# Kernel optimization log

Measured on AMD Instinct MI355X. Metric: run time of the kernel, lower is better.

## Reference

```python
import jax, jax.numpy as jnp
import numpy as np

D = 1024       # embedding_dim
H = 16         # num_attention_heads
B = 2
S = 2048       # seq_len == context_len


def setup_inputs() -> dict:
    key = jax.random.key(0)
    k1, k2, k3 = jax.random.split(key, 3)
    X = jax.random.normal(k1, (B, S, D), dtype=jnp.float32)
    W_qkv = jax.random.normal(k2, (D, 3 * D), dtype=jnp.float32) * 0.02
    b_qkv = jnp.zeros((3 * D,), dtype=jnp.float32)
    W_out = jax.random.normal(k3, (D, D), dtype=jnp.float32) * 0.02
    b_out = jnp.zeros((D,), dtype=jnp.float32)
    return {"X": X, "W_qkv": W_qkv, "b_qkv": b_qkv, "W_out": W_out, "b_out": b_out}


def reference(X, W_qkv, b_qkv, W_out, b_out):
    b, s, d = X.shape
    hd = d // H
    # fused QKV projection (GPT-2 Conv1D == x @ W + b)
    qkv = X @ W_qkv + b_qkv                       # [b, s, 3d]
    q, k, v = jnp.split(qkv, 3, axis=2)
    # [b, h, s, hd]
    q = q.reshape(b, s, H, hd).transpose(0, 2, 1, 3)
    k = k.reshape(b, s, H, hd).transpose(0, 2, 1, 3)
    v = v.reshape(b, s, H, hd).transpose(0, 2, 1, 3)
    # NOTE: source scales by rsqrt(embedding_dim), not head_dim
    scale = 1.0 / jnp.sqrt(jnp.float32(d))
    scores = jnp.einsum("bhqd,bhkd->bhqk", q, k) * scale
    causal = jnp.tril(jnp.ones((s, s), dtype=bool))
    scores = jnp.where(causal[None, None], scores, -jnp.inf)
    # attention_dropout applied pre-softmax in source; identity at eval (p used here = 0)
    probs = jax.nn.softmax(scores, axis=-1)
    attn = jnp.einsum("bhqk,bhkd->bhqd", probs, v)
    attn = attn.transpose(0, 2, 1, 3).reshape(b, s, d)
    out = attn @ W_out + b_out                    # outwards proj; dropout eval = identity
    return out
```

## Files before the change

### kernel.cpp

```cpp
#include <hip/hip_runtime.h>

#define S_LEN 2048
#define DIM   1024
#define NHEAD 16
#define HDIM  64

typedef __attribute__((ext_vector_type(8))) short  short8;
typedef __attribute__((ext_vector_type(4))) float  floatx4;
typedef __attribute__((ext_vector_type(4))) unsigned short ushort4v;

#define Q_PRESCALE 0.045084220027780106f

__device__ inline unsigned short f2bf(float f) {
  unsigned v = __builtin_bit_cast(unsigned, f);
  v += 0x7FFFu + ((v >> 16) & 1u);
  return (unsigned short)(v >> 16);
}

__device__ inline void async16(const unsigned short* g, unsigned short* l) {
  __builtin_amdgcn_global_load_lds(
      (const __attribute__((address_space(1))) unsigned int*)g,
      (__attribute__((address_space(3))) unsigned int*)l, 16, 0, 0);
}

__global__ __launch_bounds__(256) void cvt_kernel(
    const float* __restrict__ in, unsigned short* __restrict__ out, int n) {
  int i = (blockIdx.x * 256 + threadIdx.x) * 8;
  if (i >= n) return;
  float4 a = *(const float4*)&in[i];
  float4 b = *(const float4*)&in[i + 4];
  short8 o;
  o[0] = (short)f2bf(a.x); o[1] = (short)f2bf(a.y);
  o[2] = (short)f2bf(a.z); o[3] = (short)f2bf(a.w);
  o[4] = (short)f2bf(b.x); o[5] = (short)f2bf(b.y);
  o[6] = (short)f2bf(b.z); o[7] = (short)f2bf(b.w);
  *(short8*)&out[i] = o;
}

__global__ __launch_bounds__(256) void cvtT_kernel(
    const float* __restrict__ in, unsigned short* __restrict__ out, int K, int N) {
  __shared__ unsigned short tile[32][33];
  int n0 = blockIdx.x * 32, k0 = blockIdx.y * 32;
  int tx = threadIdx.x, ty = threadIdx.y;
#pragma unroll
  for (int i = 0; i < 32; i += 8)
    tile[ty + i][tx] = f2bf(in[(size_t)(k0 + ty + i) * N + n0 + tx]);
  __syncthreads();
#pragma unroll
  for (int i = 0; i < 32; i += 8)
    out[(size_t)(n0 + ty + i) * K + k0 + tx] = tile[tx][ty + i];
}

#define GEMM128_BODY(APTR, BPTR)                                                   \
  __shared__ __align__(16) unsigned short As[128][64];                             \
  __shared__ __align__(16) unsigned short Bs[128][64];                             \
  const int m0 = blockIdx.y * 128, n0 = blockIdx.x * 128;                          \
  const int t = threadIdx.x, lane = t & 63, wave = t >> 6;                         \
  const int quad = lane >> 4, l16 = lane & 15;                                     \
  const int wm = (wave >> 1) * 64, wn = (wave & 1) * 64;                           \
  const int lr = lane >> 3, lc = lane & 7, sc8 = (lc ^ lr) * 8;                    \
  const int sw = l16 & 7;                                                          \
  const int pA0 = (quad ^ sw) * 8, pA1 = ((4 + quad) ^ sw) * 8;                    \
  floatx4 acc[4][4];                                                               \
  _Pragma("unroll") for (int mi = 0; mi < 4; mi++)                                 \
      _Pragma("unroll") for (int ni = 0; ni < 4; ni++)                             \
          acc[mi][ni] = (floatx4){0.f, 0.f, 0.f, 0.f};                             \
  for (int k0 = 0; k0 < DIM; k0 += 64) {                                           \
    _Pragma("unroll") for (int i = 0; i < 4; i++) {                                \
      int rb = wave * 32 + i * 8;                                                  \
      async16(&APTR[(size_t)(m0 + rb + lr) * DIM + k0 + sc8], &As[rb][0]);         \
      async16(&BPTR[(size_t)(n0 + rb + lr) * DIM + k0 + sc8], &Bs[rb][0]);         \
    }                                                                              \
    __syncthreads();                                                               \
    short8 a0[4], a1[4];                                                           \
    _Pragma("unroll") for (int mi = 0; mi < 4; mi++) {                             \
      int row = wm + mi * 16 + l16;                                                \
      a0[mi] = *(const short8*)&As[row][pA0];                                      \
      a1[mi] = *(const short8*)&As[row][pA1];                                      \
    }                                                                              \
    _Pragma("unroll") for (int ni = 0; ni < 4; ni++) {                             \
      int row = wn + ni * 16 + l16;                                                \
      short8 b0 = *(const short8*)&Bs[row][pA0];                                   \
      short8 b1 = *(const short8*)&Bs[row][pA1];                                   \
      _Pragma("unroll") for (int mi = 0; mi < 4; mi++) {                           \
        acc[mi][ni] = __builtin_amdgcn_mfma_f32_16x16x32_bf16(a0[mi], b0, acc[mi][ni], 0, 0, 0); \
        acc[mi][ni] = __builtin_amdgcn_mfma_f32_16x16x32_bf16(a1[mi], b1, acc[mi][ni], 0, 0, 0); \
      }                                                                            \
    }                                                                              \
    __syncthreads();                                                               \
  }

__global__ __launch_bounds__(256) void gemm_qkv128(
    const unsigned short* __restrict__ Xb,
    const unsigned short* __restrict__ Wt,
    const float* __restrict__ bias,
    unsigned short* __restrict__ Qg,
    unsigned short* __restrict__ Kg,
    unsigned short* __restrict__ Vgt) {
  GEMM128_BODY(Xb, Wt)
  const int section = n0 >> 10;
  const int head = ((n0 + wn) >> 6) & 15;
#pragma unroll
  for (int mi = 0; mi < 4; mi++) {
    int mg = m0 + wm + mi * 16 + quad * 4;
    int bb = mg >> 11, sb = mg & 2047;
    size_t y = (size_t)bb * NHEAD + head;
    if (section == 2) {
#pragma unroll
      for (int ni = 0; ni < 4; ni++) {
        int hdi = ni * 16 + l16;
        float bv = bias[n0 + wn + hdi];
        ushort4v o;
#pragma unroll
        for (int r = 0; r < 4; r++) o[r] = f2bf(acc[mi][ni][r] + bv);
        *(ushort4v*)&Vgt[(y * HDIM + hdi) * S_LEN + sb] = o;
      }
    } else if (section == 0) {
#pragma unroll
      for (int ni = 0; ni < 4; ni++) {
        int hdi = ni * 16 + l16;
        float bv = bias[n0 + wn + hdi];
#pragma unroll
        for (int r = 0; r < 4; r++)
          Qg[(y * S_LEN + sb + r) * HDIM + hdi] = f2bf((acc[mi][ni][r] + bv) * Q_PRESCALE);
      }
    } else {
#pragma unroll
      for (int ni = 0; ni < 4; ni++) {
        int hdi = ni * 16 + l16;
        float bv = bias[n0 + wn + hdi];
#pragma unroll
        for (int r = 0; r < 4; r++)
          Kg[(y * S_LEN + sb + r) * HDIM + hdi] = f2bf(acc[mi][ni][r] + bv);
      }
    }
  }
}

__global__ __launch_bounds__(256) void gemm_out128(
    const unsigned short* __restrict__ A,
    const unsigned short* __restrict__ Wt,
    const float* __restrict__ bias,
    float* __restrict__ outp) {
  GEMM128_BODY(A, Wt)
#pragma unroll
  for (int ni = 0; ni < 4; ni++) {
    int n = n0 + wn + ni * 16 + l16;
    float bv = bias[n];
#pragma unroll
    for (int mi = 0; mi < 4; mi++) {
      int mg = m0 + wm + mi * 16 + quad * 4;
#pragma unroll
      for (int r = 0; r < 4; r++)
        outp[(size_t)(mg + r) * DIM + n] = acc[mi][ni][r] + bv;
    }
  }
}

__global__ __launch_bounds__(256) void gemm_qkv_kernel(
    const float* __restrict__ X,
    const unsigned short* __restrict__ Wt,
    const float* __restrict__ bias,
    unsigned short* __restrict__ Qg,
    unsigned short* __restrict__ Kg,
    unsigned short* __restrict__ Vgt,
    int g0, int G) {
  __shared__ __align__(16) unsigned short As[64][72];
  __shared__ __align__(16) unsigned short Bs[64][72];
  const int tn = blockIdx.x;
  const int section = tn / G, within = tn % G;
  const int n0 = section * 1024 + (g0 + within) * 64;
  const int m0 = blockIdx.y * 64;
  const int t = threadIdx.x, lane = t & 63, wave = t >> 6;
  const int quad = lane >> 4, l16 = lane & 15;

  floatx4 acc[4];
#pragma unroll
  for (int i = 0; i < 4; i++) acc[i] = (floatx4){0.f, 0.f, 0.f, 0.f};

  for (int k0 = 0; k0 < DIM; k0 += 64) {
#pragma unroll
    for (int i = 0; i < 2; i++) {
      int v = t + i * 256;
      int row = v >> 3, cc = (v & 7) * 8;
      float4 f0 = *(const float4*)&X[(size_t)(m0 + row) * DIM + k0 + cc];
      float4 f1 = *(const float4*)&X[(size_t)(m0 + row) * DIM + k0 + cc + 4];
      short8 o;
      o[0] = (short)f2bf(f0.x); o[1] = (short)f2bf(f0.y);
      o[2] = (short)f2bf(f0.z); o[3] = (short)f2bf(f0.w);
      o[4] = (short)f2bf(f1.x); o[5] = (short)f2bf(f1.y);
      o[6] = (short)f2bf(f1.z); o[7] = (short)f2bf(f1.w);
      *(short8*)&As[row][cc] = o;
      *(short8*)&Bs[row][cc] = *(const short8*)&Wt[(size_t)(n0 + row) * DIM + k0 + cc];
    }
    __syncthreads();
    short8 a0 = *(const short8*)&As[wave * 16 + l16][quad * 8];
    short8 a1 = *(const short8*)&As[wave * 16 + l16][32 + quad * 8];
#pragma unroll
    for (int nt = 0; nt < 4; nt++) {
      short8 b0 = *(const short8*)&Bs[nt * 16 + l16][quad * 8];
      short8 b1 = *(const short8*)&Bs[nt * 16 + l16][32 + quad * 8];
      acc[nt] = __builtin_amdgcn_mfma_f32_16x16x32_bf16(a0, b0, acc[nt], 0, 0, 0);
      acc[nt] = __builtin_amdgcn_mfma_f32_16x16x32_bf16(a1, b1, acc[nt], 0, 0, 0);
    }
    __syncthreads();
  }

  const int mbase = m0 + wave * 16 + quad * 4;
  const int b = mbase >> 11, sbase = mbase & 2047;
  const int y = b * G + within;
  if (section == 2) {
#pragma unroll
    for (int nt = 0; nt < 4; nt++) {
      int hdi = nt * 16 + l16;
      float bv = bias[n0 + hdi];
      ushort4v o;
#pragma unroll
      for (int r = 0; r < 4; r++) o[r] = f2bf(acc[nt][r] + bv);
      *(ushort4v*)&Vgt[((size_t)y * HDIM + hdi) * S_LEN + sbase] = o;
    }
  } else if (section == 0) {
#pragma unroll
    for (int nt = 0; nt < 4; nt++) {
      int hdi = nt * 16 + l16;
      float bv = bias[n0 + hdi];
#pragma unroll
      for (int r = 0; r < 4; r++)
        Qg[((size_t)y * S_LEN + sbase + r) * HDIM + hdi] =
            f2bf((acc[nt][r] + bv) * Q_PRESCALE);
    }
  } else {
#pragma unroll
    for (int nt = 0; nt < 4; nt++) {
      int hdi = nt * 16 + l16;
      float bv = bias[n0 + hdi];
#pragma unroll
      for (int r = 0; r < 4; r++)
        Kg[((size_t)y * S_LEN + sbase + r) * HDIM + hdi] = f2bf(acc[nt][r] + bv);
    }
  }
}

__global__ __launch_bounds__(256) void attn_kernel(
    const unsigned short* __restrict__ Qg,
    const unsigned short* __restrict__ Kg,
    const unsigned short* __restrict__ Vgt,
    unsigned short* __restrict__ attnB,
    int g0, int G) {
  __shared__ __align__(16) unsigned short Ks[64][72];
  __shared__ __align__(16) unsigned short Vt[80][72];
  __shared__ __align__(16) unsigned short Ps[4][16][72];

  const int y = blockIdx.y;
  const int b = y / G, hl = y % G;
  const int pairIdx = blockIdx.x;
  const int t = threadIdx.x;
  const int lane = t & 63, wave = t >> 6;
  const int quad = lane >> 4, l16 = lane & 15;

  const unsigned short* Qh = Qg + (size_t)y * S_LEN * HDIM;
  const unsigned short* Kh = Kg + (size_t)y * S_LEN * HDIM;
  const unsigned short* Vh = Vgt + (size_t)y * HDIM * S_LEN;

  {
    int rr = t >> 4, cb = (t & 15) * 4;
    ushort4v ov;
    unsigned short vv = (rr == 0) ? (unsigned short)0x3F80 : (unsigned short)0;
    ov[0] = vv; ov[1] = vv; ov[2] = vv; ov[3] = vv;
    *(ushort4v*)&Vt[64 + rr][cb] = ov;
  }

#pragma unroll
  for (int pass = 0; pass < 2; pass++) {
    const int qt = (pass == 0) ? pairIdx : (31 - pairIdx);
    const int q0 = qt * 64;

    short8 aq0 = *(const short8*)&Qh[(size_t)(q0 + wave * 16 + l16) * HDIM + quad * 8];
    short8 aq1 = *(const short8*)&Qh[(size_t)(q0 + wave * 16 + l16) * HDIM + 32 + quad * 8];

    floatx4 o_acc[5];
#pragma unroll
    for (int dt = 0; dt < 5; dt++) o_acc[dt] = (floatx4){0.f, 0.f, 0.f, 0.f};

    for (int j0 = 0; j0 <= q0; j0 += 64) {
#pragma unroll
      for (int i = 0; i < 2; i++) {
        int v = t + i * 256;
        int row = v >> 3, cc = (v & 7) * 8;
        *(short8*)&Ks[row][cc] = *(const short8*)&Kh[(size_t)(j0 + row) * HDIM + cc];
        *(short8*)&Vt[row][cc] = *(const short8*)&Vh[(size_t)row * S_LEN + j0 + cc];
      }
      __syncthreads();

      floatx4 sc[4];
#pragma unroll
      for (int nt = 0; nt < 4; nt++) {
        sc[nt] = (floatx4){0.f, 0.f, 0.f, 0.f};
        short8 b0 = *(const short8*)&Ks[nt * 16 + l16][quad * 8];
        short8 b1 = *(const short8*)&Ks[nt * 16 + l16][32 + quad * 8];
        sc[nt] = __builtin_amdgcn_mfma_f32_16x16x32_bf16(aq0, b0, sc[nt], 0, 0, 0);
        sc[nt] = __builtin_amdgcn_mfma_f32_16x16x32_bf16(aq1, b1, sc[nt], 0, 0, 0);
      }

      if (j0 == q0) {
#pragma unroll
        for (int nt = 0; nt < 4; nt++) {
          int keyl = nt * 16 + l16;
#pragma unroll
          for (int r = 0; r < 4; r++) {
            int ql = wave * 16 + quad * 4 + r;
            float p = exp2f(sc[nt][r]);
            p = (keyl <= ql) ? p : 0.f;
            Ps[wave][quad * 4 + r][nt * 16 + l16] = f2bf(p);
          }
        }
      } else {
#pragma unroll
        for (int nt = 0; nt < 4; nt++) {
#pragma unroll
          for (int r = 0; r < 4; r++)
            Ps[wave][quad * 4 + r][nt * 16 + l16] = f2bf(exp2f(sc[nt][r]));
        }
      }
      short8 ap0 = *(const short8*)&Ps[wave][l16][quad * 8];
      short8 ap1 = *(const short8*)&Ps[wave][l16][32 + quad * 8];

#pragma unroll
      for (int dt = 0; dt < 5; dt++) {
        short8 bv0 = *(const short8*)&Vt[dt * 16 + l16][quad * 8];
        short8 bv1 = *(const short8*)&Vt[dt * 16 + l16][32 + quad * 8];
        o_acc[dt] = __builtin_amdgcn_mfma_f32_16x16x32_bf16(ap0, bv0, o_acc[dt], 0, 0, 0);
        o_acc[dt] = __builtin_amdgcn_mfma_f32_16x16x32_bf16(ap1, bv1, o_acc[dt], 0, 0, 0);
      }
      __syncthreads();
    }

    float linv[4];
#pragma unroll
    for (int r = 0; r < 4; r++)
      linv[r] = 1.0f / __shfl(o_acc[4][r], quad << 4);

#pragma unroll
    for (int dt = 0; dt < 4; dt++) {
#pragma unroll
      for (int r = 0; r < 4; r++) {
        int qg = q0 + wave * 16 + quad * 4 + r;
        attnB[(size_t)(b * S_LEN + qg) * DIM + (g0 + hl) * HDIM + dt * 16 + l16] =
            f2bf(o_acc[dt][r] * linv[r]);
      }
    }
  }
}

extern "C" void kernel_launch(void* const* d_in, const int* in_sizes, int n_in,
                              void* d_out, int out_size, void* d_ws, size_t ws_size,
                              hipStream_t stream) {
  const float* X    = (const float*)d_in[0];
  const float* Wqkv = (const float*)d_in[1];
  const float* bqkv = (const float*)d_in[2];
  const float* Wout = (const float*)d_in[3];
  const float* bout = (const float*)d_in[4];
  float* outp = (float*)d_out;

  unsigned short* Wqkvt = (unsigned short*)d_ws;
  unsigned short* Woutt = Wqkvt + (size_t)3145728;
  unsigned short* attnB = Woutt + (size_t)1048576;
  unsigned short* Qg    = attnB + (size_t)4194304;
  unsigned short* Kg    = Qg + (size_t)4194304;
  unsigned short* Vgt   = Kg + (size_t)4194304;
  unsigned short* Xb    = Vgt + (size_t)4194304;

  const bool bigWs = ws_size >= (size_t)48 * 1024 * 1024;

  cvtT_kernel<<<dim3(3072 / 32, 1024 / 32), dim3(32, 8), 0, stream>>>(Wqkv, Wqkvt, 1024, 3072);
  cvtT_kernel<<<dim3(1024 / 32, 1024 / 32), dim3(32, 8), 0, stream>>>(Wout, Woutt, 1024, 1024);

  if (bigWs) {
    cvt_kernel<<<4194304 / (256 * 8), 256, 0, stream>>>(X, Xb, 4194304);
    gemm_qkv128<<<dim3(3072 / 128, 4096 / 128), 256, 0, stream>>>(
        Xb, Wqkvt, bqkv, Qg, Kg, Vgt);
  } else {
    gemm_qkv_kernel<<<dim3(48, 64), 256, 0, stream>>>(
        X, Wqkvt, bqkv, Qg, Kg, Vgt, 0, 16);
  }
  attn_kernel<<<dim3(16, 32), 256, 0, stream>>>(Qg, Kg, Vgt, attnB, 0, 16);
  gemm_out128<<<dim3(1024 / 128, 4096 / 128), 256, 0, stream>>>(attnB, Woutt, bout, outp);
}
```

Before: 206.7 us.

## Double-buffer K/V with async LDS loads and 128-row query tiles in attention

Restructures the attention kernel to process 128 query rows per pass, so each K/V tile loaded into LDS is reused by two 64-row sub-tiles. K/V tiles are prefetched with global_load_lds into double buffers using an XOR-swizzled layout, which overlaps loading with MFMA work and avoids bank conflicts. K/V fragments are hoisted into registers once per tile. The grid is halved to 8x32 blocks, which lowers parallelism and raises register pressure.

```diff
diff --git a/kernel.cpp b/kernel.cpp
--- a/kernel.cpp
+++ b/kernel.cpp
@@ -245,108 +245,155 @@
     const unsigned short* __restrict__ Qg,
     const unsigned short* __restrict__ Kg,
     const unsigned short* __restrict__ Vgt,
-    unsigned short* __restrict__ attnB,
-    int g0, int G) {
-  __shared__ __align__(16) unsigned short Ks[64][72];
-  __shared__ __align__(16) unsigned short Vt[80][72];
-  __shared__ __align__(16) unsigned short Ps[4][16][72];
+    unsigned short* __restrict__ attnB) {
+  __shared__ __align__(16) unsigned short Ks[2][64][64];
+  __shared__ __align__(16) unsigned short Vs[2][64][64];
+  __shared__ __align__(16) unsigned short Ones[16][64];
+  __shared__ __align__(16) unsigned short Ps[4][32][72];
 
   const int y = blockIdx.y;
-  const int b = y / G, hl = y % G;
+  const int b = y >> 4, h = y & 15;
   const int pairIdx = blockIdx.x;
   const int t = threadIdx.x;
   const int lane = t & 63, wave = t >> 6;
   const int quad = lane >> 4, l16 = lane & 15;
+  const int lr = lane >> 3, lc = lane & 7;
+  const int sc8 = (lc ^ lr) * 8;
+  const int sw = l16 & 7;
+  const int p0 = (quad ^ sw) * 8, p1 = ((4 + quad) ^ sw) * 8;
 
   const unsigned short* Qh = Qg + (size_t)y * S_LEN * HDIM;
   const unsigned short* Kh = Kg + (size_t)y * S_LEN * HDIM;
   const unsigned short* Vh = Vgt + (size_t)y * HDIM * S_LEN;
 
-  {
-    int rr = t >> 4, cb = (t & 15) * 4;
-    ushort4v ov;
-    unsigned short vv = (rr == 0) ? (unsigned short)0x3F80 : (unsigned short)0;
-    ov[0] = vv; ov[1] = vv; ov[2] = vv; ov[3] = vv;
-    *(ushort4v*)&Vt[64 + rr][cb] = ov;
+  if (t < 128) {
+    int row = t >> 3, c = (t & 7) * 8;
+    unsigned short vv = (row == 0) ? (unsigned short)0x3F80 : (unsigned short)0;
+    short8 o;
+#pragma unroll
+    for (int j = 0; j < 8; j++) o[j] = (short)vv;
+    *(short8*)&Ones[row][c] = o;
   }
 
 #pragma unroll
   for (int pass = 0; pass < 2; pass++) {
-    const int qt = (pass == 0) ? pairIdx : (31 - pairIdx);
-    const int q0 = qt * 64;
-
-    short8 aq0 = *(const short8*)&Qh[(size_t)(q0 + wave * 16 + l16) * HDIM + quad * 8];
-    short8 aq1 = *(const short8*)&Qh[(size_t)(q0 + wave * 16 + l16) * HDIM + 32 + quad * 8];
-
-    floatx4 o_acc[5];
-#pragma unroll
-    for (int dt = 0; dt < 5; dt++) o_acc[dt] = (floatx4){0.f, 0.f, 0.f, 0.f};
-
-    for (int j0 = 0; j0 <= q0; j0 += 64) {
+    const int qb = pass ? (15 - pairIdx) : pairIdx;
+    const int q0 = qb * 128;
+    const int nT = (q0 >> 6) + 2;
+
+    short8 aq[2][2];
+#pragma unroll
+    for (int mi = 0; mi < 2; mi++) {
+      const unsigned short* qp = &Qh[(size_t)(q0 + mi * 64 + wave * 16 + l16) * HDIM];
+      aq[mi][0] = *(const short8*)&qp[quad * 8];
+      aq[mi][1] = *(const short8*)&qp[32 + quad * 8];
+    }
+
+    floatx4 o_acc[2][5];
+#pragma unroll
+    for (int mi = 0; mi < 2; mi++)
+#pragma unroll
+      for (int dt = 0; dt < 5; dt++) o_acc[mi][dt] = (floatx4){0.f, 0.f, 0.f, 0.f};
+
+    __syncthreads();
+    {
+      int rb = wave * 16;
 #pragma unroll
       for (int i = 0; i < 2; i++) {
-        int v = t + i * 256;
-        int row = v >> 3, cc = (v & 7) * 8;
-        *(short8*)&Ks[row][cc] = *(const short8*)&Kh[(size_t)(j0 + row) * HDIM + cc];
-        *(short8*)&Vt[row][cc] = *(const short8*)&Vh[(size_t)row * S_LEN + j0 + cc];
-      }
+        async16(&Kh[(size_t)(rb + i * 8 + lr) * HDIM + sc8], &Ks[0][rb + i * 8][0]);
+        async16(&Vh[(size_t)(rb + i * 8 + lr) * S_LEN + sc8], &Vs[0][rb + i * 8][0]);
+      }
+    }
+
+    for (int tt = 0; tt < nT; tt++) {
+      const int j0 = tt * 64;
+      const int buf = tt & 1;
       __syncthreads();
-
-      floatx4 sc[4];
+      if (tt + 1 < nT) {
+        int j1 = j0 + 64, nb = 1 - buf;
+        int rb = wave * 16;
+#pragma unroll
+        for (int i = 0; i < 2; i++) {
+          async16(&Kh[(size_t)(j1 + rb + i * 8 + lr) * HDIM + sc8], &Ks[nb][rb + i * 8][0]);
+          async16(&Vh[(size_t)(rb + i * 8 + lr) * S_LEN + j1 + sc8], &Vs[nb][rb + i * 8][0]);
+        }
+      }
+
+      short8 kb0[4], kb1[4];
 #pragma unroll
       for (int nt = 0; nt < 4; nt++) {
-        sc[nt] = (floatx4){0.f, 0.f, 0.f, 0.f};
-        short8 b0 = *(const short8*)&Ks[nt * 16 + l16][quad * 8];
-        short8 b1 = *(const short8*)&Ks[nt * 16 + l16][32 + quad * 8];
-        sc[nt] = __builtin_amdgcn_mfma_f32_16x16x32_bf16(aq0, b0, sc[nt], 0, 0, 0);
-        sc[nt] = __builtin_amdgcn_mfma_f32_16x16x32_bf16(aq1, b1, sc[nt], 0, 0, 0);
-      }
-
-      if (j0 == q0) {
+        kb0[nt] = *(const short8*)&Ks[buf][nt * 16 + l16][p0];
+        kb1[nt] = *(const short8*)&Ks[buf][nt * 16 + l16][p1];
+      }
+
+#pragma unroll
+      for (int mi = 0; mi < 2; mi++) {
+        if (j0 > q0 + mi * 64 + 63) continue;
+        floatx4 sc[4];
 #pragma unroll
         for (int nt = 0; nt < 4; nt++) {
-          int keyl = nt * 16 + l16;
-#pragma unroll
-          for (int r = 0; r < 4; r++) {
-            int ql = wave * 16 + quad * 4 + r;
-            float p = exp2f(sc[nt][r]);
-            p = (keyl <= ql) ? p : 0.f;
-            Ps[wave][quad * 4 + r][nt * 16 + l16] = f2bf(p);
+          sc[nt] = (floatx4){0.f, 0.f, 0.f, 0.f};
+          sc[nt] = __builtin_amdgcn_mfma_f32_16x16x32_bf16(aq[mi][0], kb0[nt], sc[nt], 0, 0, 0);
+          sc[nt] = __builtin_amdgcn_mfma_f32_16x16x32_bf16(aq[mi][1], kb1[nt], sc[nt], 0, 0, 0);
+        }
+        const int W0 = q0 + mi * 64 + wave * 16;
+        if (j0 + 63 <= W0) {
+#pragma unroll
+          for (int nt = 0; nt < 4; nt++)
+#pragma unroll
+            for (int r = 0; r < 4; r++)
+              Ps[wave][mi * 16 + quad * 4 + r][nt * 16 + l16] = f2bf(exp2f(sc[nt][r]));
+        } else {
+#pragma unroll
+          for (int nt = 0; nt < 4; nt++) {
+            int keyg = j0 + nt * 16 + l16;
+#pragma unroll
+            for (int r = 0; r < 4; r++) {
+              int qg = W0 + quad * 4 + r;
+              float p = exp2f(sc[nt][r]);
+              p = (keyg <= qg) ? p : 0.f;
+              Ps[wave][mi * 16 + quad * 4 + r][nt * 16 + l16] = f2bf(p);
+            }
           }
         }
-      } else {
-#pragma unroll
-        for (int nt = 0; nt < 4; nt++) {
-#pragma unroll
-          for (int r = 0; r < 4; r++)
-            Ps[wave][quad * 4 + r][nt * 16 + l16] = f2bf(exp2f(sc[nt][r]));
+      }
+
+      short8 vb0[5], vb1[5];
+#pragma unroll
+      for (int dt = 0; dt < 4; dt++) {
+        vb0[dt] = *(const short8*)&Vs[buf][dt * 16 + l16][p0];
+        vb1[dt] = *(const short8*)&Vs[buf][dt * 16 + l16][p1];
+      }
+      vb0[4] = *(const short8*)&Ones[l16][p0];
+      vb1[4] = *(const short8*)&Ones[l16][p1];
+
+#pragma unroll
+      for (int mi = 0; mi < 2; mi++) {
+        if (j0 > q0 + mi * 64 + 63) continue;
+        short8 ap0 = *(const short8*)&Ps[wave][mi * 16 + l16][quad * 8];
+        short8 ap1 = *(const short8*)&Ps[wave][mi * 16 + l16][32 + quad * 8];
+#pragma unroll
+        for (int dt = 0; dt < 5; dt++) {
+          o_acc[mi][dt] = __builtin_amdgcn_mfma_f32_16x16x32_bf16(ap0, vb0[dt], o_acc[mi][dt], 0, 0, 0);
+          o_acc[mi][dt] = __builtin_amdgcn_mfma_f32_16x16x32_bf16(ap1, vb1[dt], o_acc[mi][dt], 0, 0, 0);
         }
       }
-      short8 ap0 = *(const short8*)&Ps[wave][l16][quad * 8];
-      short8 ap1 = *(const short8*)&Ps[wave][l16][32 + quad * 8];
-
-#pragma unroll
-      for (int dt = 0; dt < 5; dt++) {
-        short8 bv0 = *(const short8*)&Vt[dt * 16 + l16][quad * 8];
-        short8 bv1 = *(const short8*)&Vt[dt * 16 + l16][32 + quad * 8];
-        o_acc[dt] = __builtin_amdgcn_mfma_f32_16x16x32_bf16(ap0, bv0, o_acc[dt], 0, 0, 0);
-        o_acc[dt] = __builtin_amdgcn_mfma_f32_16x16x32_bf16(ap1, bv1, o_acc[dt], 0, 0, 0);
-      }
-      __syncthreads();
-    }
-
-    float linv[4];
-#pragma unroll
-    for (int r = 0; r < 4; r++)
-      linv[r] = 1.0f / __shfl(o_acc[4][r], quad << 4);
-
-#pragma unroll
-    for (int dt = 0; dt < 4; dt++) {
-#pragma unroll
-      for (int r = 0; r < 4; r++) {
-        int qg = q0 + wave * 16 + quad * 4 + r;
-        attnB[(size_t)(b * S_LEN + qg) * DIM + (g0 + hl) * HDIM + dt * 16 + l16] =
-            f2bf(o_acc[dt][r] * linv[r]);
+    }
+
+#pragma unroll
+    for (int mi = 0; mi < 2; mi++) {
+      float linv[4];
+#pragma unroll
+      for (int r = 0; r < 4; r++)
+        linv[r] = 1.0f / __shfl(o_acc[mi][4][r], quad << 4);
+#pragma unroll
+      for (int dt = 0; dt < 4; dt++) {
+#pragma unroll
+        for (int r = 0; r < 4; r++) {
+          int qg = q0 + mi * 64 + wave * 16 + quad * 4 + r;
+          attnB[(size_t)(b * S_LEN + qg) * DIM + h * HDIM + dt * 16 + l16] =
+              f2bf(o_acc[mi][dt][r] * linv[r]);
+        }
       }
     }
   }
@@ -383,6 +430,6 @@
     gemm_qkv_kernel<<<dim3(48, 64), 256, 0, stream>>>(
         X, Wqkvt, bqkv, Qg, Kg, Vgt, 0, 16);
   }
-  attn_kernel<<<dim3(16, 32), 256, 0, stream>>>(Qg, Kg, Vgt, attnB, 0, 16);
+  attn_kernel<<<dim3(8, 32), 256, 0, stream>>>(Qg, Kg, Vgt, attnB);
   gemm_out128<<<dim3(1024 / 128, 4096 / 128), 256, 0, stream>>>(attnB, Woutt, bout, outp);
 }
```

After: 221.1 us. 1.07x slower.

## Double-buffer K/V tiles with async LDS loads and one query tile per block

Applied to the files above, without the earlier changes.

The attention kernel now prefetches the next K and V tiles into a second shared-memory buffer through global_load_lds while the current tile is computed, and applies an XOR swizzle to the LDS columns in place of padding. It also launches one block per query tile, heaviest tiles first, instead of pairing a short and a long tile in each block, which doubles the grid. The ones row used for the row-sum moves to its own small LDS array. The intent is to hide global load latency and cut bank conflicts, at the cost of more LDS and a less even per-block workload.

```diff
diff --git a/kernel.cpp b/kernel.cpp
--- a/kernel.cpp
+++ b/kernel.cpp
@@ -245,109 +245,126 @@
     const unsigned short* __restrict__ Qg,
     const unsigned short* __restrict__ Kg,
     const unsigned short* __restrict__ Vgt,
-    unsigned short* __restrict__ attnB,
-    int g0, int G) {
-  __shared__ __align__(16) unsigned short Ks[64][72];
-  __shared__ __align__(16) unsigned short Vt[80][72];
+    unsigned short* __restrict__ attnB) {
+  __shared__ __align__(16) unsigned short Ks[2][64][64];
+  __shared__ __align__(16) unsigned short Vs[2][64][64];
+  __shared__ __align__(16) unsigned short Ones[16][64];
   __shared__ __align__(16) unsigned short Ps[4][16][72];
 
-  const int y = blockIdx.y;
-  const int b = y / G, hl = y % G;
-  const int pairIdx = blockIdx.x;
+  const int y = blockIdx.x;
+  const int b = y >> 4, h = y & 15;
+  const int qt = 31 - blockIdx.y;
+  const int q0 = qt * 64;
+  const int nT = qt + 1;
   const int t = threadIdx.x;
   const int lane = t & 63, wave = t >> 6;
   const int quad = lane >> 4, l16 = lane & 15;
+  const int lr = lane >> 3, lc = lane & 7;
+  const int sc8 = (lc ^ lr) * 8;
+  const int sw = l16 & 7;
+  const int p0 = (quad ^ sw) * 8, p1 = ((4 + quad) ^ sw) * 8;
 
   const unsigned short* Qh = Qg + (size_t)y * S_LEN * HDIM;
   const unsigned short* Kh = Kg + (size_t)y * S_LEN * HDIM;
   const unsigned short* Vh = Vgt + (size_t)y * HDIM * S_LEN;
 
+  if (t < 128) {
+    int row = t >> 3, c = (t & 7) * 8;
+    unsigned short vv = (row == 0) ? (unsigned short)0x3F80 : (unsigned short)0;
+    short8 o;
+#pragma unroll
+    for (int j = 0; j < 8; j++) o[j] = (short)vv;
+    *(short8*)&Ones[row][c] = o;
+  }
+
+  short8 aq0, aq1;
   {
-    int rr = t >> 4, cb = (t & 15) * 4;
-    ushort4v ov;
-    unsigned short vv = (rr == 0) ? (unsigned short)0x3F80 : (unsigned short)0;
-    ov[0] = vv; ov[1] = vv; ov[2] = vv; ov[3] = vv;
-    *(ushort4v*)&Vt[64 + rr][cb] = ov;
-  }
-
-#pragma unroll
-  for (int pass = 0; pass < 2; pass++) {
-    const int qt = (pass == 0) ? pairIdx : (31 - pairIdx);
-    const int q0 = qt * 64;
-
-    short8 aq0 = *(const short8*)&Qh[(size_t)(q0 + wave * 16 + l16) * HDIM + quad * 8];
-    short8 aq1 = *(const short8*)&Qh[(size_t)(q0 + wave * 16 + l16) * HDIM + 32 + quad * 8];
-
-    floatx4 o_acc[5];
-#pragma unroll
-    for (int dt = 0; dt < 5; dt++) o_acc[dt] = (floatx4){0.f, 0.f, 0.f, 0.f};
-
-    for (int j0 = 0; j0 <= q0; j0 += 64) {
+    const unsigned short* qp = &Qh[(size_t)(q0 + wave * 16 + l16) * HDIM];
+    aq0 = *(const short8*)&qp[quad * 8];
+    aq1 = *(const short8*)&qp[32 + quad * 8];
+  }
+
+  floatx4 o_acc[5];
+#pragma unroll
+  for (int dt = 0; dt < 5; dt++) o_acc[dt] = (floatx4){0.f, 0.f, 0.f, 0.f};
+
+  {
+    int rb = wave * 16;
+#pragma unroll
+    for (int i = 0; i < 2; i++) {
+      async16(&Kh[(size_t)(rb + i * 8 + lr) * HDIM + sc8], &Ks[0][rb + i * 8][0]);
+      async16(&Vh[(size_t)(rb + i * 8 + lr) * S_LEN + sc8], &Vs[0][rb + i * 8][0]);
+    }
+  }
+
+  for (int tt = 0; tt < nT; tt++) {
+    const int j0 = tt * 64;
+    const int buf = tt & 1;
+    __syncthreads();
+    if (tt + 1 < nT) {
+      int j1 = j0 + 64, nb = 1 - buf;
+      int rb = wave * 16;
 #pragma unroll
       for (int i = 0; i < 2; i++) {
-        int v = t + i * 256;
-        int row = v >> 3, cc = (v & 7) * 8;
-        *(short8*)&Ks[row][cc] = *(const short8*)&Kh[(size_t)(j0 + row) * HDIM + cc];
-        *(short8*)&Vt[row][cc] = *(const short8*)&Vh[(size_t)row * S_LEN + j0 + cc];
+        async16(&Kh[(size_t)(j1 + rb + i * 8 + lr) * HDIM + sc8], &Ks[nb][rb + i * 8][0]);
+        async16(&Vh[(size_t)(rb + i * 8 + lr) * S_LEN + j1 + sc8], &Vs[nb][rb + i * 8][0]);
       }
-      __syncthreads();
-
-      floatx4 sc[4];
+    }
+
+    floatx4 sc[4];
+#pragma unroll
+    for (int nt = 0; nt < 4; nt++) {
+      short8 kb0 = *(const short8*)&Ks[buf][nt * 16 + l16][p0];
+      short8 kb1 = *(const short8*)&Ks[buf][nt * 16 + l16][p1];
+      sc[nt] = (floatx4){0.f, 0.f, 0.f, 0.f};
+      sc[nt] = __builtin_amdgcn_mfma_f32_16x16x32_bf16(aq0, kb0, sc[nt], 0, 0, 0);
+      sc[nt] = __builtin_amdgcn_mfma_f32_16x16x32_bf16(aq1, kb1, sc[nt], 0, 0, 0);
+    }
+
+    if (j0 == q0) {
 #pragma unroll
       for (int nt = 0; nt < 4; nt++) {
-        sc[nt] = (floatx4){0.f, 0.f, 0.f, 0.f};
-        short8 b0 = *(const short8*)&Ks[nt * 16 + l16][quad * 8];
-        short8 b1 = *(const short8*)&Ks[nt * 16 + l16][32 + quad * 8];
-        sc[nt] = __builtin_amdgcn_mfma_f32_16x16x32_bf16(aq0, b0, sc[nt], 0, 0, 0);
-        sc[nt] = __builtin_amdgcn_mfma_f32_16x16x32_bf16(aq1, b1, sc[nt], 0, 0, 0);
-      }
-
-      if (j0 == q0) {
-#pragma unroll
-        for (int nt = 0; nt < 4; nt++) {
-          int keyl = nt * 16 + l16;
-#pragma unroll
-          for (int r = 0; r < 4; r++) {
-            int ql = wave * 16 + quad * 4 + r;
-            float p = exp2f(sc[nt][r]);
-            p = (keyl <= ql) ? p : 0.f;
-            Ps[wave][quad * 4 + r][nt * 16 + l16] = f2bf(p);
-          }
-        }
-      } else {
-#pragma unroll
-        for (int nt = 0; nt < 4; nt++) {
-#pragma unroll
-          for (int r = 0; r < 4; r++)
-            Ps[wave][quad * 4 + r][nt * 16 + l16] = f2bf(exp2f(sc[nt][r]));
+        int keyl = nt * 16 + l16;
+#pragma unroll
+        for (int r = 0; r < 4; r++) {
+          int ql = wave * 16 + quad * 4 + r;
+          float p = exp2f(sc[nt][r]);
+          p = (keyl <= ql) ? p : 0.f;
+          Ps[wave][quad * 4 + r][nt * 16 + l16] = f2bf(p);
         }
       }
-      short8 ap0 = *(const short8*)&Ps[wave][l16][quad * 8];
-      short8 ap1 = *(const short8*)&Ps[wave][l16][32 + quad * 8];
-
-#pragma unroll
-      for (int dt = 0; dt < 5; dt++) {
-        short8 bv0 = *(const short8*)&Vt[dt * 16 + l16][quad * 8];
-        short8 bv1 = *(const short8*)&Vt[dt * 16 + l16][32 + quad * 8];
-        o_acc[dt] = __builtin_amdgcn_mfma_f32_16x16x32_bf16(ap0, bv0, o_acc[dt], 0, 0, 0);
-        o_acc[dt] = __builtin_amdgcn_mfma_f32_16x16x32_bf16(ap1, bv1, o_acc[dt], 0, 0, 0);
-      }
-      __syncthreads();
-    }
-
-    float linv[4];
-#pragma unroll
-    for (int r = 0; r < 4; r++)
-      linv[r] = 1.0f / __shfl(o_acc[4][r], quad << 4);
-
-#pragma unroll
-    for (int dt = 0; dt < 4; dt++) {
-#pragma unroll
-      for (int r = 0; r < 4; r++) {
-        int qg = q0 + wave * 16 + quad * 4 + r;
-        attnB[(size_t)(b * S_LEN + qg) * DIM + (g0 + hl) * HDIM + dt * 16 + l16] =
-            f2bf(o_acc[dt][r] * linv[r]);
-      }
+    } else {
+#pragma unroll
+      for (int nt = 0; nt < 4; nt++)
+#pragma unroll
+        for (int r = 0; r < 4; r++)
+          Ps[wave][quad * 4 + r][nt * 16 + l16] = f2bf(exp2f(sc[nt][r]));
+    }
+    short8 ap0 = *(const short8*)&Ps[wave][l16][quad * 8];
+    short8 ap1 = *(const short8*)&Ps[wave][l16][32 + quad * 8];
+
+#pragma unroll
+    for (int dt = 0; dt < 5; dt++) {
+      short8 vb0 = (dt < 4) ? *(const short8*)&Vs[buf][dt * 16 + l16][p0]
+                            : *(const short8*)&Ones[l16][p0];
+      short8 vb1 = (dt < 4) ? *(const short8*)&Vs[buf][dt * 16 + l16][p1]
+                            : *(const short8*)&Ones[l16][p1];
+      o_acc[dt] = __builtin_amdgcn_mfma_f32_16x16x32_bf16(ap0, vb0, o_acc[dt], 0, 0, 0);
+      o_acc[dt] = __builtin_amdgcn_mfma_f32_16x16x32_bf16(ap1, vb1, o_acc[dt], 0, 0, 0);
+    }
+  }
+
+  float linv[4];
+#pragma unroll
+  for (int r = 0; r < 4; r++)
+    linv[r] = 1.0f / __shfl(o_acc[4][r], quad << 4);
+#pragma unroll
+  for (int dt = 0; dt < 4; dt++) {
+#pragma unroll
+    for (int r = 0; r < 4; r++) {
+      int qg = q0 + wave * 16 + quad * 4 + r;
+      attnB[(size_t)(b * S_LEN + qg) * DIM + h * HDIM + dt * 16 + l16] =
+          f2bf(o_acc[dt][r] * linv[r]);
     }
   }
 }
@@ -383,6 +400,6 @@
     gemm_qkv_kernel<<<dim3(48, 64), 256, 0, stream>>>(
         X, Wqkvt, bqkv, Qg, Kg, Vgt, 0, 16);
   }
-  attn_kernel<<<dim3(16, 32), 256, 0, stream>>>(Qg, Kg, Vgt, attnB, 0, 16);
+  attn_kernel<<<dim3(32, 32), 256, 0, stream>>>(Qg, Kg, Vgt, attnB);
   gemm_out128<<<dim3(1024 / 128, 4096 / 128), 256, 0, stream>>>(attnB, Woutt, bout, outp);
 }
```

After: 193.8 us. 1.07x faster.
